# Optimization experiments

Hardware: AMD Instinct MI355X
Metric: run time of the kernel (lower is better)

## Reference

```python
import jax, jax.numpy as jnp
import numpy as np

N_NODES = 100000
N_EDGES = 3200000
N_GRAPHS = 1000


def setup_inputs() -> dict:
    key = jax.random.key(0)
    ks = jax.random.split(key, 12)
    inp = {
        "x": jax.random.normal(ks[0], (N_NODES, 4), dtype=jnp.float32),
        "W1": jax.random.normal(ks[1], (4, 64), dtype=jnp.float32) * 0.5,
        "b1": jax.random.normal(ks[2], (64,), dtype=jnp.float32) * 0.1,
        "W2": jax.random.normal(ks[3], (64, 32), dtype=jnp.float32) * 0.125,
        "b2": jax.random.normal(ks[4], (32,), dtype=jnp.float32) * 0.1,
        "W3": jax.random.normal(ks[5], (32, 16), dtype=jnp.float32) * 0.17,
        "b3": jax.random.normal(ks[6], (16,), dtype=jnp.float32) * 0.1,
        "Wl": jax.random.normal(ks[7], (16, 1), dtype=jnp.float32) * 0.25,
        "bl": jax.random.normal(ks[8], (1,), dtype=jnp.float32) * 0.1,
        "edge_index": jax.random.randint(ks[9], (2, N_EDGES), 0, N_NODES, dtype=jnp.int32),
        "batch": jnp.sort(jax.random.randint(ks[10], (N_NODES,), 0, N_GRAPHS, dtype=jnp.int32)),
    }
    return inp


def _gcn_conv(h, W, b, src, dst, norm, num_nodes):
    # PyG GCNConv: transform, then normalized scatter-add over edges (incl. self-loops)
    h = h @ W                                    # [N, out]
    msg = h[src] * norm[:, None]                 # [E+N, out]
    out = jax.ops.segment_sum(msg, dst, num_segments=num_nodes)
    return out + b


def reference(x, W1, b1, W2, b2, W3, b3, Wl, bl, edge_index, batch):
    num_nodes = x.shape[0]
    num_graphs = N_GRAPHS
    loop = jnp.arange(num_nodes, dtype=edge_index.dtype)
    src = jnp.concatenate([edge_index[0], loop])  # edges + self-loops
    dst = jnp.concatenate([edge_index[1], loop])
    # symmetric degree normalization: deg over destination incl. self-loops
    deg = jax.ops.segment_sum(jnp.ones_like(dst, dtype=x.dtype), dst, num_segments=num_nodes)
    dinv = jnp.where(deg > 0, jax.lax.rsqrt(deg), 0.0)
    norm = dinv[src] * dinv[dst]                 # [E+N]

    h = jax.nn.relu(_gcn_conv(x, W1, b1, src, dst, norm, num_nodes))
    h = jax.nn.relu(_gcn_conv(h, W2, b2, src, dst, norm, num_nodes))
    h = _gcn_conv(h, W3, b3, src, dst, norm, num_nodes)

    # global_mean_pool
    sums = jax.ops.segment_sum(h, batch, num_segments=num_graphs)        # [G,16]
    cnts = jax.ops.segment_sum(jnp.ones((num_nodes,), x.dtype), batch, num_segments=num_graphs)
    pooled = sums / jnp.maximum(cnts, 1.0)[:, None]

    return jax.nn.relu(pooled @ Wl + bl)          # [G,1]
```

## Files before the change

### kernel.cpp

```cpp
#include <hip/hip_runtime.h>
#include <hip/hip_fp16.h>

#define N_NODES 100000
#define N_EDGES 3200000
#define N_GRAPHS 1000
#define NB 1024
#define NPB 98
#define CAP 3584
#define EPB 4096
#define EPT 16


__global__ void k_zero(int* __restrict__ bcnt) {
    int i = blockIdx.x * blockDim.x + threadIdx.x;
    if (i < NB) bcnt[i] = 0;
}

__global__ __launch_bounds__(256) void k_bucket(
    const int* __restrict__ src, const int* __restrict__ dst,
    int* __restrict__ bcnt, unsigned* __restrict__ pay) {
    __shared__ int cnt[NB];
    __shared__ int off[NB];
    __shared__ int scanbuf[256];
    __shared__ unsigned rec[EPB];

    int tid = threadIdx.x;
    int e0 = blockIdx.x * EPB;
    for (int i = tid; i < NB; i += 256) cnt[i] = 0;
    __syncthreads();

    unsigned wreg[EPT], breg[EPT];
#pragma unroll
    for (int k = 0; k < EPT; ++k) {
        int e = e0 + k * 256 + tid;
        if (e < N_EDGES) {
            unsigned s = (unsigned)src[e];
            unsigned d = (unsigned)dst[e];
            unsigned b = d / NPB;
            unsigned ld = d - b * NPB;
            wreg[k] = s | (ld << 17);
            breg[k] = b;
            atomicAdd(&cnt[b], 1);
        } else {
            breg[k] = 0xFFFFFFFFu;
        }
    }
    __syncthreads();

    int base = tid * 4;
    int c0 = cnt[base], c1 = cnt[base + 1], c2 = cnt[base + 2], c3 = cnt[base + 3];
    int part = c0 + c1 + c2 + c3;
    scanbuf[tid] = part;
    __syncthreads();
    for (int o = 1; o < 256; o <<= 1) {
        int v = (tid >= o) ? scanbuf[tid - o] : 0;
        __syncthreads();
        scanbuf[tid] += v;
        __syncthreads();
    }
    int ex = scanbuf[tid] - part;
    off[base]     = ex;
    off[base + 1] = ex + c0;
    off[base + 2] = ex + c0 + c1;
    off[base + 3] = ex + c0 + c1 + c2;
    __syncthreads();

#pragma unroll
    for (int k = 0; k < EPT; ++k) {
        if (breg[k] != 0xFFFFFFFFu) {
            int p = atomicAdd(&off[breg[k]], 1);
            rec[p] = wreg[k];
        }
    }
    __syncthreads();

    for (int b = tid; b < NB; b += 256) {
        int c = cnt[b];
        if (c == 0) continue;
        int ls = off[b] - c;
        int gb = atomicAdd(&bcnt[b], c);
        unsigned* dstp = pay + (size_t)b * CAP;
        for (int k = 0; k < c; ++k) {
            int gp = gb + k;
            if (gp < CAP) dstp[gp] = rec[ls + k];
        }
    }
}

__global__ __launch_bounds__(256) void k_sort(
    unsigned* __restrict__ pay, const int* __restrict__ bcnt,
    const float* __restrict__ x, float* __restrict__ dinv,
    float* __restrict__ xp, int* __restrict__ row, int* __restrict__ dgar) {
    __shared__ unsigned rec[CAP], rec2[CAP];
    __shared__ int hl[NPB], st[NPB], ofl[NPB], sc[128];
    int tid = threadIdx.x;
    int b = blockIdx.x;
    int cnt = bcnt[b]; if (cnt > CAP) cnt = CAP;
    unsigned* P = pay + (size_t)b * CAP;

    if (tid < NPB) hl[tid] = 0;
    __syncthreads();

    for (int i = tid; i < cnt; i += 256) {
        unsigned w = P[i];
        rec[i] = w;
        atomicAdd(&hl[w >> 17], 1);
    }
    __syncthreads();

    if (tid < 128) sc[tid] = (tid < NPB) ? hl[tid] : 0;
    __syncthreads();
    for (int o = 1; o < 128; o <<= 1) {
        int v = 0;
        if (tid < 128 && tid >= o) v = sc[tid - o];
        __syncthreads();
        if (tid < 128) sc[tid] += v;
        __syncthreads();
    }
    if (tid < NPB) {
        int s = sc[tid] - hl[tid];
        st[tid] = s;
        ofl[tid] = s;
    }
    __syncthreads();

    if (tid < NPB) {
        int n = b * NPB + tid;
        if (n < N_NODES) {
            row[n]  = b * CAP + st[tid];
            dgar[n] = hl[tid];
            float di = rsqrtf((float)(hl[tid] + 1));
            dinv[n] = di;
            float4 v = reinterpret_cast<const float4*>(x)[n];
            v.x *= di; v.y *= di; v.z *= di; v.w *= di;
            reinterpret_cast<float4*>(xp)[n] = v;
        }
    }
    __syncthreads();

    for (int i = tid; i < cnt; i += 256) {
        unsigned w = rec[i];
        int p = atomicAdd(&ofl[w >> 17], 1);
        rec2[p] = w;
    }
    __syncthreads();

    for (int i = tid; i < cnt; i += 256) P[i] = rec2[i];
}

__global__ __launch_bounds__(256) void k_g1(
    const float* __restrict__ xp, const unsigned* __restrict__ pay,
    const int* __restrict__ row, const int* __restrict__ dgar,
    float* __restrict__ agg1) {
    int tid = threadIdx.x;
    int lane = tid & 3;
    int n = blockIdx.x * 64 + (tid >> 2);
    if (n >= N_NODES) return;
    int r = row[n], d = dgar[n];
    const unsigned* P = pay + r;
    float acc = 0.0f;
#pragma unroll 4
    for (int j = 0; j < d; ++j) {
        int sn = P[j] & 0x1FFFF;
        acc += xp[sn * 4 + lane];
    }
    agg1[(size_t)n * 4 + lane] = acc;
}

__global__ __launch_bounds__(256) void k_dense1(
    const float* __restrict__ agg1, const float* __restrict__ xp,
    const float* __restrict__ dinv,
    const float* __restrict__ W1, const float* __restrict__ b1,
    const float* __restrict__ W2, __half* __restrict__ t2ph) {
    __shared__ float sW1[256], sb1[64], sW2[2048];
    int tid = threadIdx.x;
    sW1[tid] = W1[tid];
    if (tid < 64) sb1[tid] = b1[tid];
    for (int i = tid; i < 2048; i += 256) sW2[i] = W2[i];
    __syncthreads();

    int n = blockIdx.x * 256 + tid;
    if (n >= N_NODES) return;
    float di = dinv[n];
    float4 ag = reinterpret_cast<const float4*>(agg1)[n];
    float4 sv = reinterpret_cast<const float4*>(xp)[n];
    float a[4] = {(ag.x + sv.x) * di, (ag.y + sv.y) * di,
                  (ag.z + sv.z) * di, (ag.w + sv.w) * di};
    float t[32];
#pragma unroll
    for (int k = 0; k < 32; ++k) t[k] = 0.0f;
    for (int j = 0; j < 64; ++j) {
        float h = sb1[j];
#pragma unroll
        for (int i = 0; i < 4; ++i) h += a[i] * sW1[i * 64 + j];
        h = fmaxf(h, 0.0f);
#pragma unroll
        for (int k = 0; k < 32; ++k) t[k] += h * sW2[j * 32 + k];
    }
    __half2* o = reinterpret_cast<__half2*>(t2ph + (size_t)n * 32);
#pragma unroll
    for (int q = 0; q < 16; ++q)
        o[q] = __floats2half2_rn(t[2*q] * di, t[2*q+1] * di);
}

__global__ __launch_bounds__(256) void k_g2(
    const __half* __restrict__ t2ph, const unsigned* __restrict__ pay,
    const int* __restrict__ row, const int* __restrict__ dgar,
    float* __restrict__ agg2) {
    int tid = threadIdx.x;
    int lane = tid & 3;
    int n = blockIdx.x * 64 + (tid >> 2);
    if (n >= N_NODES) return;
    int r = row[n], d = dgar[n];
    const unsigned* P = pay + r;
    float a0 = 0, a1 = 0, a2 = 0, a3 = 0, a4 = 0, a5 = 0, a6 = 0, a7 = 0;
#pragma unroll 4
    for (int j = 0; j < d; ++j) {
        int sn = P[j] & 0x1FFFF;
        union { uint4 u; __half2 h[4]; } U;
        U.u = *reinterpret_cast<const uint4*>(t2ph + (size_t)sn * 32 + lane * 8);
        float2 f0 = __half22float2(U.h[0]);
        float2 f1 = __half22float2(U.h[1]);
        float2 f2 = __half22float2(U.h[2]);
        float2 f3 = __half22float2(U.h[3]);
        a0 += f0.x; a1 += f0.y; a2 += f1.x; a3 += f1.y;
        a4 += f2.x; a5 += f2.y; a6 += f3.x; a7 += f3.y;
    }
    float4* o = reinterpret_cast<float4*>(agg2 + (size_t)n * 32 + lane * 8);
    o[0] = make_float4(a0, a1, a2, a3);
    o[1] = make_float4(a4, a5, a6, a7);
}

__global__ __launch_bounds__(256) void k_dense2(
    const float* __restrict__ agg2, const __half* __restrict__ t2ph,
    const float* __restrict__ dinv,
    const float* __restrict__ b2, const float* __restrict__ W3,
    __half* __restrict__ t3ph) {
    __shared__ float sb2[32], sW3[512];
    int tid = threadIdx.x;
    if (tid < 32) sb2[tid] = b2[tid];
    for (int i = tid; i < 512; i += 256) sW3[i] = W3[i];
    __syncthreads();

    int n = blockIdx.x * 256 + tid;
    if (n >= N_NODES) return;
    float di = dinv[n];
    const float2* ag = reinterpret_cast<const float2*>(agg2 + (size_t)n * 32);
    const __half2* sp = reinterpret_cast<const __half2*>(t2ph + (size_t)n * 32);
    float h[32];
#pragma unroll
    for (int q = 0; q < 16; ++q) {
        float2 a = ag[q];
        float2 sv = __half22float2(sp[q]);
        h[2*q]   = fmaxf((a.x + sv.x) * di + sb2[2*q],   0.0f);
        h[2*q+1] = fmaxf((a.y + sv.y) * di + sb2[2*q+1], 0.0f);
    }
    float t[16];
#pragma unroll
    for (int k = 0; k < 16; ++k) t[k] = 0.0f;
    for (int j = 0; j < 32; ++j) {
#pragma unroll
        for (int k = 0; k < 16; ++k) t[k] += h[j] * sW3[j * 16 + k];
    }
    __half2* o = reinterpret_cast<__half2*>(t3ph + (size_t)n * 16);
#pragma unroll
    for (int q = 0; q < 8; ++q)
        o[q] = __floats2half2_rn(t[2*q] * di, t[2*q+1] * di);
}

__global__ __launch_bounds__(256) void k_g3(
    const __half* __restrict__ t3ph, const unsigned* __restrict__ pay,
    const int* __restrict__ row, const int* __restrict__ dgar,
    const float* __restrict__ dinv, const float* __restrict__ b3,
    const float* __restrict__ Wl, float* __restrict__ sval) {
    int tid = threadIdx.x;
    int lane = tid & 3;
    int n = blockIdx.x * 64 + (tid >> 2);
    if (n >= N_NODES) return;
    int r = row[n], d = dgar[n];
    const unsigned* P = pay + r;
    float a0 = 0, a1 = 0, a2 = 0, a3 = 0;
#pragma unroll 4
    for (int j = 0; j < d; ++j) {
        int sn = P[j] & 0x1FFFF;
        union { uint2 u; __half2 h[2]; } U;
        U.u = *reinterpret_cast<const uint2*>(t3ph + (size_t)sn * 16 + lane * 4);
        float2 f0 = __half22float2(U.h[0]);
        float2 f1 = __half22float2(U.h[1]);
        a0 += f0.x; a1 += f0.y; a2 += f1.x; a3 += f1.y;
    }
    union { uint2 u; __half2 h[2]; } S;
    S.u = *reinterpret_cast<const uint2*>(t3ph + (size_t)n * 16 + lane * 4);
    float2 s0 = __half22float2(S.h[0]);
    float2 s1 = __half22float2(S.h[1]);
    float di = dinv[n];
    float p = ((a0 + s0.x) * di + b3[lane * 4 + 0]) * Wl[lane * 4 + 0]
            + ((a1 + s0.y) * di + b3[lane * 4 + 1]) * Wl[lane * 4 + 1]
            + ((a2 + s1.x) * di + b3[lane * 4 + 2]) * Wl[lane * 4 + 2]
            + ((a3 + s1.y) * di + b3[lane * 4 + 3]) * Wl[lane * 4 + 3];
    p += __shfl_xor(p, 1);
    p += __shfl_xor(p, 2);
    if (lane == 0) sval[n] = p;
}

__global__ __launch_bounds__(64) void k_poolg(
    const float* __restrict__ sval, const int* __restrict__ batch,
    const float* __restrict__ bl, float* __restrict__ out) {
    int g = blockIdx.x;
    int lo = 0, hi = N_NODES;
    while (lo < hi) { int m = (lo + hi) >> 1; if (batch[m] < g) lo = m + 1; else hi = m; }
    int s0 = lo;
    hi = N_NODES;
    while (lo < hi) { int m = (lo + hi) >> 1; if (batch[m] < g + 1) lo = m + 1; else hi = m; }
    int s1 = lo;
    float s = 0.0f;
    for (int i = s0 + threadIdx.x; i < s1; i += 64) s += sval[i];
#pragma unroll
    for (int o = 32; o > 0; o >>= 1) s += __shfl_down(s, o);
    if (threadIdx.x == 0) {
        float c = fmaxf((float)(s1 - s0), 1.0f);
        out[g] = fmaxf(s / c + bl[0], 0.0f);
    }
}

extern "C" void kernel_launch(void* const* d_in, const int* in_sizes, int n_in,
                              void* d_out, int out_size, void* d_ws, size_t ws_size,
                              hipStream_t stream) {
    const float* x  = (const float*)d_in[0];
    const float* W1 = (const float*)d_in[1];
    const float* b1 = (const float*)d_in[2];
    const float* W2 = (const float*)d_in[3];
    const float* b2 = (const float*)d_in[4];
    const float* W3 = (const float*)d_in[5];
    const float* b3 = (const float*)d_in[6];
    const float* Wl = (const float*)d_in[7];
    const float* bl = (const float*)d_in[8];
    const int*   ei = (const int*)d_in[9];
    const int* batch = (const int*)d_in[10];
    const int* src = ei;
    const int* dst = ei + N_EDGES;
    float* out = (float*)d_out;

    const size_t N = N_NODES;
    char* ws = (char*)d_ws;
    float*    dinv = (float*)   (ws);
    float*    xp   = (float*)   (ws + 4 * (N));
    __half*   t2ph = (__half*)  (ws + 4 * (5 * N));
    __half*   t3ph = (__half*)  (ws + 4 * (21 * N));
    float*    agg1 = (float*)   (ws + 4 * (29 * N));
    float*    agg2 = (float*)   (ws + 4 * (33 * N));
    float*    sval = (float*)   (ws + 4 * (65 * N));
    int*      row  = (int*)     (ws + 4 * (81 * N));
    int*      dgar = (int*)     (ws + 4 * (82 * N));
    int*      bcnt = (int*)     (ws + 4 * (83 * N));
    unsigned* pay  = (unsigned*)(ws + 4 * (83 * N + NB));

    const int B = 256;
    const int gN = (N_NODES + B - 1) / B;
    const int gB = (N_EDGES + EPB - 1) / EPB;
    const int gG = (N_NODES + 63) / 64;

    k_zero  <<<(NB + B - 1) / B, B, 0, stream>>>(bcnt);
    k_bucket<<<gB, B, 0, stream>>>(src, dst, bcnt, pay);
    k_sort  <<<NB, B, 0, stream>>>(pay, bcnt, x, dinv, xp, row, dgar);
    k_g1    <<<gG, B, 0, stream>>>(xp, pay, row, dgar, agg1);
    k_dense1<<<gN, B, 0, stream>>>(agg1, xp, dinv, W1, b1, W2, t2ph);
    k_g2    <<<gG, B, 0, stream>>>(t2ph, pay, row, dgar, agg2);
    k_dense2<<<gN, B, 0, stream>>>(agg2, t2ph, dinv, b2, W3, t3ph);
    k_g3    <<<gG, B, 0, stream>>>(t3ph, pay, row, dgar, dinv, b3, Wl, sval);
    k_poolg <<<N_GRAPHS, 64, 0, stream>>>(sval, batch, bl, out);
}
```

Baseline: 282.5 us.

## Sub-sort edges within each node by source chunk and double edges per bucket block

The per-bucket sort now keys each edge by destination node and by one of eight source-index chunks, so every node's incoming edges are grouped by source range. The aim is better cache locality for the later gather passes that read source features. The bucketing kernel also processes twice as many edges per block (EPB 4096→8192, EPT 16→32). The cost is a larger shared-memory histogram and scan, plus an integer division per edge in the sort kernel.

```diff
diff --git a/kernel.cpp b/kernel.cpp
--- a/kernel.cpp
+++ b/kernel.cpp
@@ -7,8 +7,11 @@
 #define NB 1024
 #define NPB 98
 #define CAP 3584
-#define EPB 4096
-#define EPT 16
+#define EPB 8192
+#define EPT 32
+#define NCH 8
+#define CHN 12500
+#define PBINS (NPB * NCH)
 
 
 __global__ void k_zero(int* __restrict__ bcnt) {
@@ -92,44 +95,60 @@
     const float* __restrict__ x, float* __restrict__ dinv,
     float* __restrict__ xp, int* __restrict__ row, int* __restrict__ dgar) {
     __shared__ unsigned rec[CAP], rec2[CAP];
-    __shared__ int hl[NPB], st[NPB], ofl[NPB], sc[128];
+    __shared__ int cnb[PBINS], exl[PBINS], ofl[PBINS];
+    __shared__ int scanbuf[256];
     int tid = threadIdx.x;
     int b = blockIdx.x;
     int cnt = bcnt[b]; if (cnt > CAP) cnt = CAP;
     unsigned* P = pay + (size_t)b * CAP;
 
-    if (tid < NPB) hl[tid] = 0;
+    for (int i = tid; i < PBINS; i += 256) cnb[i] = 0;
     __syncthreads();
 
     for (int i = tid; i < cnt; i += 256) {
         unsigned w = P[i];
         rec[i] = w;
-        atomicAdd(&hl[w >> 17], 1);
-    }
-    __syncthreads();
-
-    if (tid < 128) sc[tid] = (tid < NPB) ? hl[tid] : 0;
-    __syncthreads();
-    for (int o = 1; o < 128; o <<= 1) {
-        int v = 0;
-        if (tid < 128 && tid >= o) v = sc[tid - o];
+        int key = (int)(w >> 17) * NCH + (int)((w & 0x1FFFF) / CHN);
+        atomicAdd(&cnb[key], 1);
+    }
+    __syncthreads();
+
+    int part = 0, c0 = 0, c1 = 0, c2 = 0, c3 = 0;
+    int base = tid * 4;
+    if (base < PBINS) {
+        c0 = cnb[base]; c1 = cnb[base + 1]; c2 = cnb[base + 2]; c3 = cnb[base + 3];
+        part = c0 + c1 + c2 + c3;
+    }
+    scanbuf[tid] = part;
+    __syncthreads();
+    for (int o = 1; o < 256; o <<= 1) {
+        int v = (tid >= o) ? scanbuf[tid - o] : 0;
         __syncthreads();
-        if (tid < 128) sc[tid] += v;
+        scanbuf[tid] += v;
         __syncthreads();
     }
-    if (tid < NPB) {
-        int s = sc[tid] - hl[tid];
-        st[tid] = s;
-        ofl[tid] = s;
+    if (base < PBINS) {
+        int ex = scanbuf[tid] - part;
+        exl[base]     = ex;
+        exl[base + 1] = ex + c0;
+        exl[base + 2] = ex + c0 + c1;
+        exl[base + 3] = ex + c0 + c1 + c2;
+        ofl[base]     = exl[base];
+        ofl[base + 1] = exl[base + 1];
+        ofl[base + 2] = exl[base + 2];
+        ofl[base + 3] = exl[base + 3];
     }
     __syncthreads();
 
     if (tid < NPB) {
         int n = b * NPB + tid;
         if (n < N_NODES) {
-            row[n]  = b * CAP + st[tid];
-            dgar[n] = hl[tid];
-            float di = rsqrtf((float)(hl[tid] + 1));
+            int s0 = exl[tid * NCH];
+            int s1 = exl[tid * NCH + NCH - 1] + cnb[tid * NCH + NCH - 1];
+            row[n]  = b * CAP + s0;
+            int dg  = s1 - s0;
+            dgar[n] = dg;
+            float di = rsqrtf((float)(dg + 1));
             dinv[n] = di;
             float4 v = reinterpret_cast<const float4*>(x)[n];
             v.x *= di; v.y *= di; v.z *= di; v.w *= di;
@@ -140,7 +159,8 @@
 
     for (int i = tid; i < cnt; i += 256) {
         unsigned w = rec[i];
-        int p = atomicAdd(&ofl[w >> 17], 1);
+        int key = (int)(w >> 17) * NCH + (int)((w & 0x1FFFF) / CHN);
+        int p = atomicAdd(&ofl[key], 1);
         rec2[p] = w;
     }
     __syncthreads();
```

After: 252.9 us. -10.5%, faster.
